# Performance work log

Measured on AMD Instinct MI355X. Metric: run time of the kernel, lower is better.

Reference implementation:

```python
import jax, jax.numpy as jnp
import numpy as np
from jax import lax

SMOOTH = 1e-06
SKEL_ITERS = 10  # thresh_width in the original soft_skeletonize


def _maxpool3(x):
    # 3x3 max pool, stride 1, padding 1 on NCHW
    return lax.reduce_window(
        x, -jnp.inf, lax.max,
        window_dimensions=(1, 1, 3, 3),
        window_strides=(1, 1, 1, 1),
        padding=((0, 0), (0, 0), (1, 1), (1, 1)))


def soft_skeletonize(x):
    def body(i, x):
        min_pool_x = -_maxpool3(-x)                      # 3x3 min-pool (erosion)
        contour = jax.nn.relu(_maxpool3(min_pool_x) - min_pool_x)
        return jax.nn.relu(x - contour)
    return lax.fori_loop(0, SKEL_ITERS, body, x)


def norm_intersection(center_line, vessel):
    B, C = center_line.shape[:2]
    clf = center_line.reshape(B, C, -1)
    vf = vessel.reshape(B, C, -1)
    intersection = jnp.sum(clf * vf, axis=-1)
    return (intersection + SMOOTH) / (jnp.sum(clf, axis=-1) + SMOOTH)


def setup_inputs() -> dict:
    key = jax.random.key(0)
    k1, k2 = jax.random.split(key)
    B, C, H, W = 32, 1, 512, 512
    pred = jax.random.uniform(k1, (B, C, H, W), dtype=jnp.float32)
    target = (jax.random.uniform(k2, (B, C, H, W), dtype=jnp.float32) > 0.85).astype(jnp.float32)
    return {"pred": pred, "target": target}


def reference(pred, target):
    cl_pred = soft_skeletonize(pred)
    target_skeleton = soft_skeletonize(target)
    iflat = norm_intersection(cl_pred, target)
    tflat = norm_intersection(target_skeleton, pred)
    intersection = jnp.sum(iflat * tflat)
    return 1.0 - 2.0 * intersection / jnp.sum(iflat + tflat)
```

## Files before the change

### kernel.cpp

```cpp
#include <hip/hip_runtime.h>
#include <hip/hip_fp16.h>
#include <math.h>

#define HH 512
#define WW 512
#define BB 32
#define CHUNK 32

typedef unsigned u32;

#define NEG_INF2 0xFC00FC00u
#define POS_INF2 0x7C007C00u

__device__ __forceinline__ u32 pkmin(u32 a, u32 b) {
    u32 r; asm("v_pk_min_f16 %0, %1, %2" : "=v"(r) : "v"(a), "v"(b)); return r;
}
__device__ __forceinline__ u32 pkmax(u32 a, u32 b) {
    u32 r; asm("v_pk_max_f16 %0, %1, %2" : "=v"(r) : "v"(a), "v"(b)); return r;
}
__device__ __forceinline__ u32 pksub(u32 a, u32 b) {
    u32 r; asm("v_pk_add_f16 %0, %1, %2 neg_lo:[0,1] neg_hi:[0,1]" : "=v"(r) : "v"(a), "v"(b)); return r;
}
__device__ __forceinline__ u32 min3p(u32 a, u32 b, u32 c) { return pkmin(pkmin(a, b), c); }
__device__ __forceinline__ u32 max3p(u32 a, u32 b, u32 c) { return pkmax(pkmax(a, b), c); }

__device__ __forceinline__ u32 shl1(u32 a, u32 b) {
    return __builtin_amdgcn_alignbit(b, a, 16);
}

union H2U { __half2 h; u32 u; };
__device__ __forceinline__ u32 f2toh2(float lo, float hi) {
    H2U t; t.h = __float22half2_rn(make_float2(lo, hi)); return t.u;
}
__device__ __forceinline__ float2 h2tof2(u32 v) {
    H2U t; t.u = v; return __half22float2(t.h);
}

template <int F32>
__device__ __forceinline__ void loadrow6(const float* __restrict__ imgF,
                                         const unsigned short* __restrict__ imgH,
                                         int R, int cm4, int c0, int cp4,
                                         bool isL, bool isR, u32* X) {
    const int Rc = R < 0 ? 0 : (R > HH - 1 ? HH - 1 : R);
    if (F32) {
        const float* rb = imgF + (size_t)Rc * WW;
        float4 v0 = *(const float4*)(rb + cm4);
        float4 v1 = *(const float4*)(rb + c0);
        float4 v2 = *(const float4*)(rb + cp4);
        X[0] = f2toh2(v0.x, v0.y); X[1] = f2toh2(v0.z, v0.w);
        X[2] = f2toh2(v1.x, v1.y); X[3] = f2toh2(v1.z, v1.w);
        X[4] = f2toh2(v2.x, v2.y); X[5] = f2toh2(v2.z, v2.w);
    } else {
        const unsigned short* rb = imgH + (size_t)Rc * WW;
        uint2 a = *(const uint2*)(rb + cm4);
        uint2 b = *(const uint2*)(rb + c0);
        uint2 c = *(const uint2*)(rb + cp4);
        X[0] = a.x; X[1] = a.y; X[2] = b.x; X[3] = b.y; X[4] = c.x; X[5] = c.y;
    }
    u32 fl = __builtin_amdgcn_perm(X[0], X[1], 0x05040100u);
    X[1] = isL ? fl : X[1];
    u32 fr = __builtin_amdgcn_perm(X[4], X[3], 0x07060302u);
    X[4] = isR ? fr : X[4];
}

template <int SRCF32, int FUSED>
__device__ __forceinline__ void rowstep(
    const float* __restrict__ imgF, const unsigned short* __restrict__ imgH,
    const float* __restrict__ cmp, unsigned short* __restrict__ outp,
    float& acc0, float& acc1,
    int R, int cm4, int gx0, int cp4, bool isL, bool isR, bool doStore,
    u32 (&X)[6], u32 (&XL)[6],
    u32 (&hm0o)[6], u32 (&hm0n)[6], u32 (&mn0p)[4],
    u32 (&hx0o)[4], u32 (&hx0n)[4],
    u32 (&x0o)[4], u32 (&x0n)[4],
    u32 (&hm1o)[4], u32 (&hm1n)[4], u32 (&mn1p)[2],
    u32 (&hx1o)[2], u32 (&hx1n)[2],
    u32 (&x1o)[2], u32 (&x1n)[2],
    const u32 (&mk)[8],
    float4& cqC, float4& cqL) {
    loadrow6<SRCF32>(imgF, imgH, R + 3, cm4, gx0, cp4, isL, isR, XL);

    float4 cmpCur;
    if (FUSED) {
        cmpCur = cqC;
        int Rc = R - 1;
        Rc = Rc < 0 ? 0 : (Rc > HH - 1 ? HH - 1 : Rc);
        cqL = *(const float4*)(cmp + (size_t)Rc * WW + gx0);
    }

    u32 L[7];
    L[0] = shl1(X[0], X[0]);
    #pragma unroll
    for (int j = 1; j <= 5; ++j) L[j] = shl1(X[j - 1], X[j]);
    L[6] = shl1(X[5], X[5]);
    u32 hm0c[6];
    #pragma unroll
    for (int j = 0; j < 6; ++j) hm0c[j] = min3p(L[j], X[j], L[j + 1]);

    u32 M[6];
    #pragma unroll
    for (int j = 0; j < 6; ++j) M[j] = min3p(hm0o[j], hm0n[j], hm0c[j]);
    if (!((unsigned)(R - 1) < HH)) {
        #pragma unroll
        for (int j = 0; j < 6; ++j) M[j] = NEG_INF2;
    }
    M[0] = pkmin(M[0], mk[0]); M[1] = pkmin(M[1], mk[1]);
    M[4] = pkmin(M[4], mk[2]); M[5] = pkmin(M[5], mk[3]);

    u32 ML[6];
    #pragma unroll
    for (int j = 1; j <= 5; ++j) ML[j] = shl1(M[j - 1], M[j]);
    u32 hx0c[4];
    #pragma unroll
    for (int j = 0; j < 4; ++j) hx0c[j] = max3p(ML[j + 1], M[j + 1], ML[j + 2]);

    u32 x1c[4];
    #pragma unroll
    for (int j = 0; j < 4; ++j) {
        u32 mp = max3p(hx0o[j], hx0n[j], hx0c[j]);
        u32 ct = pkmax(pksub(mp, mn0p[j]), 0u);
        x1c[j] = pkmax(pksub(x0o[j], ct), 0u);
    }
    if (!((unsigned)(R - 2) < HH)) {
        #pragma unroll
        for (int j = 0; j < 4; ++j) x1c[j] = POS_INF2;
    }
    x1c[0] = pkmax(x1c[0], mk[4]);
    x1c[3] = pkmax(x1c[3], mk[5]);

    #pragma unroll
    for (int j = 0; j < 6; ++j) hm0o[j] = hm0c[j];
    #pragma unroll
    for (int j = 0; j < 4; ++j) { mn0p[j] = M[j + 1]; hx0o[j] = hx0c[j]; x0o[j] = X[j + 1]; }

    u32 XL1[5];
    XL1[0] = shl1(x1c[0], x1c[0]);
    #pragma unroll
    for (int j = 1; j <= 3; ++j) XL1[j] = shl1(x1c[j - 1], x1c[j]);
    XL1[4] = shl1(x1c[3], x1c[3]);
    u32 hm1c[4];
    #pragma unroll
    for (int j = 0; j < 4; ++j) hm1c[j] = min3p(XL1[j], x1c[j], XL1[j + 1]);

    u32 M1[4];
    #pragma unroll
    for (int j = 0; j < 4; ++j) M1[j] = min3p(hm1o[j], hm1n[j], hm1c[j]);
    if (!((unsigned)(R - 3) < HH)) {
        #pragma unroll
        for (int j = 0; j < 4; ++j) M1[j] = NEG_INF2;
    }
    M1[0] = pkmin(M1[0], mk[6]);
    M1[3] = pkmin(M1[3], mk[7]);

    u32 M1s[4];
    #pragma unroll
    for (int j = 1; j <= 3; ++j) M1s[j] = shl1(M1[j - 1], M1[j]);
    u32 hx1c[2];
    hx1c[0] = max3p(M1s[1], M1[1], M1s[2]);
    hx1c[1] = max3p(M1s[2], M1[2], M1s[3]);

    if (doStore) {
        u32 o[2];
        #pragma unroll
        for (int k = 0; k < 2; ++k) {
            u32 mp = max3p(hx1o[k], hx1n[k], hx1c[k]);
            u32 ct = pkmax(pksub(mp, mn1p[k]), 0u);
            o[k] = pkmax(pksub(x1o[k], ct), 0u);
        }
        if (FUSED) {
            float2 f0 = h2tof2(o[0]);
            float2 f1 = h2tof2(o[1]);
            acc0 += f0.x * cmpCur.x + f0.y * cmpCur.y + f1.x * cmpCur.z + f1.y * cmpCur.w;
            acc1 += f0.x + f0.y + f1.x + f1.y;
        } else {
            uint2 ov;
            ov.x = o[0]; ov.y = o[1];
            *(uint2*)(outp + (size_t)(R - 4) * WW + gx0) = ov;
        }
    }

    #pragma unroll
    for (int j = 0; j < 4; ++j) hm1o[j] = hm1c[j];
    mn1p[0] = M1[1]; mn1p[1] = M1[2];
    hx1o[0] = hx1c[0]; hx1o[1] = hx1c[1];
    x1o[0] = x1c[1]; x1o[1] = x1c[2];
}

template <int SRCF32, int FUSED>
__global__ __launch_bounds__(256) void skel2h_t(const float* __restrict__ sfA,
                                                const float* __restrict__ sfB,
                                                const unsigned short* __restrict__ shA,
                                                const unsigned short* __restrict__ shB,
                                                const float* __restrict__ cmpA,
                                                const float* __restrict__ cmpB,
                                                unsigned short* __restrict__ dst,
                                                float* __restrict__ partials) {
    const int s = blockIdx.x * 64 + threadIdx.x;
    const int y0 = (blockIdx.y * 4 + threadIdx.y) * CHUNK;
    const int z = blockIdx.z;
    const float* imgF = nullptr;
    const unsigned short* imgH = nullptr;
    if (SRCF32) imgF = (z < BB) ? (sfA + (size_t)z * (HH * WW))
                                : (sfB + (size_t)(z - BB) * (HH * WW));
    else        imgH = (z < BB) ? (shA + (size_t)z * (HH * WW))
                                : (shB + (size_t)(z - BB) * (HH * WW));
    const float* cmp = nullptr;
    if (FUSED) cmp = (z < BB) ? (cmpA + (size_t)z * (HH * WW))
                              : (cmpB + (size_t)(z - BB) * (HH * WW));
    unsigned short* outp = FUSED ? nullptr : (dst + (size_t)z * (HH * WW));
    const int gx0 = 4 * s;
    const bool isL = (s == 0), isR = (s == 127);
    const int cm4 = isL ? 0 : gx0 - 4;
    const int cp4 = isR ? gx0 : gx0 + 4;

    u32 mk[8];
    mk[0] = isL ? 0xFC007C00u : POS_INF2;
    mk[1] = isL ? NEG_INF2    : POS_INF2;
    mk[2] = isR ? NEG_INF2    : POS_INF2;
    mk[3] = isR ? 0x7C00FC00u : POS_INF2;
    mk[4] = isL ? POS_INF2    : NEG_INF2;
    mk[5] = isR ? POS_INF2    : NEG_INF2;
    mk[6] = isL ? 0xFC007C00u : POS_INF2;
    mk[7] = isR ? 0x7C00FC00u : POS_INF2;

    u32 hm0a[6], hm0b[6], mn0p[4];
    u32 hx0a[4], hx0b[4], x0a[4], x0b[4];
    u32 hm1a[4], hm1b[4], mn1p[2];
    u32 hx1a[2], hx1b[2], x1a[2], x1b[2];
    u32 xs0[6], xs1[6], xs2[6], xs3[6];
    float4 cq0, cq1, cq2, cq3;

    #pragma unroll
    for (int j = 0; j < 6; ++j) { hm0a[j] = POS_INF2; hm0b[j] = POS_INF2; }
    #pragma unroll
    for (int j = 0; j < 4; ++j) {
        mn0p[j] = NEG_INF2; hx0a[j] = NEG_INF2; hx0b[j] = NEG_INF2;
        x0a[j] = POS_INF2; x0b[j] = POS_INF2;
        hm1a[j] = POS_INF2; hm1b[j] = POS_INF2;
    }
    #pragma unroll
    for (int k = 0; k < 2; ++k) {
        mn1p[k] = NEG_INF2; hx1a[k] = NEG_INF2; hx1b[k] = NEG_INF2;
        x1a[k] = POS_INF2; x1b[k] = POS_INF2;
    }
    cq0.x = cq0.y = cq0.z = cq0.w = 0.f;
    cq1 = cq0; cq2 = cq0; cq3 = cq0;

    float acc0 = 0.0f, acc1 = 0.0f;

    loadrow6<SRCF32>(imgF, imgH, y0 - 4, cm4, gx0, cp4, isL, isR, xs0);
    loadrow6<SRCF32>(imgF, imgH, y0 - 3, cm4, gx0, cp4, isL, isR, xs1);
    loadrow6<SRCF32>(imgF, imgH, y0 - 2, cm4, gx0, cp4, isL, isR, xs2);

    #pragma unroll 1
    for (int it = 0; it < (CHUNK + 8) / 4; ++it) {
        const int Rb = y0 - 4 + 4 * it;
        const bool doStore = (it >= 2);
        rowstep<SRCF32, FUSED>(imgF, imgH, cmp, outp, acc0, acc1,
            Rb + 0, cm4, gx0, cp4, isL, isR, doStore,
            xs0, xs3, hm0a, hm0b, mn0p, hx0a, hx0b, x0a, x0b,
            hm1a, hm1b, mn1p, hx1a, hx1b, x1a, x1b, mk, cq0, cq3);
        rowstep<SRCF32, FUSED>(imgF, imgH, cmp, outp, acc0, acc1,
            Rb + 1, cm4, gx0, cp4, isL, isR, doStore,
            xs1, xs0, hm0b, hm0a, mn0p, hx0b, hx0a, x0b, x0a,
            hm1b, hm1a, mn1p, hx1b, hx1a, x1b, x1a, mk, cq1, cq0);
        rowstep<SRCF32, FUSED>(imgF, imgH, cmp, outp, acc0, acc1,
            Rb + 2, cm4, gx0, cp4, isL, isR, doStore,
            xs2, xs1, hm0a, hm0b, mn0p, hx0a, hx0b, x0a, x0b,
            hm1a, hm1b, mn1p, hx1a, hx1b, x1a, x1b, mk, cq2, cq1);
        rowstep<SRCF32, FUSED>(imgF, imgH, cmp, outp, acc0, acc1,
            Rb + 3, cm4, gx0, cp4, isL, isR, doStore,
            xs3, xs2, hm0b, hm0a, mn0p, hx0b, hx0a, x0b, x0a,
            hm1b, hm1a, mn1p, hx1b, hx1a, x1b, x1a, mk, cq3, cq2);
    }

    if (FUSED) {
        for (int off = 32; off; off >>= 1) {
            acc0 += __shfl_down(acc0, off);
            acc1 += __shfl_down(acc1, off);
        }
        __shared__ float red[4][2];
        if (threadIdx.x == 0) { red[threadIdx.y][0] = acc0; red[threadIdx.y][1] = acc1; }
        __syncthreads();
        if (threadIdx.x == 0 && threadIdx.y == 0) {
            const int tile = blockIdx.x * gridDim.y + blockIdx.y;
            float* p = partials + ((size_t)z * 16 + tile) * 2;
            p[0] = red[0][0] + red[1][0] + red[2][0] + red[3][0];
            p[1] = red[0][1] + red[1][1] + red[2][1] + red[3][1];
        }
    }
}

__global__ __launch_bounds__(64) void finalize2(const float* __restrict__ partials,
                                                int ntiles,
                                                float* __restrict__ out) {
    const int b = threadIdx.x;
    float iflat = 0.f, tflat = 0.f;
    if (b < BB) {
        float v0 = 0.f, v1 = 0.f, v2 = 0.f, v3 = 0.f;
        for (int t = 0; t < ntiles; ++t) {
            v0 += partials[((size_t)b * 16 + t) * 2 + 0];
            v1 += partials[((size_t)b * 16 + t) * 2 + 1];
            v2 += partials[((size_t)(b + BB) * 16 + t) * 2 + 0];
            v3 += partials[((size_t)(b + BB) * 16 + t) * 2 + 1];
        }
        iflat = (v0 + 1e-6f) / (v1 + 1e-6f);
        tflat = (v2 + 1e-6f) / (v3 + 1e-6f);
    }
    float prod = iflat * tflat;
    float ssum = iflat + tflat;
    for (int off = 32; off; off >>= 1) {
        prod += __shfl_down(prod, off);
        ssum += __shfl_down(ssum, off);
    }
    if (threadIdx.x == 0) out[0] = 1.0f - 2.0f * prod / ssum;
}

extern "C" void kernel_launch(void* const* d_in, const int* in_sizes, int n_in,
                              void* d_out, int out_size, void* d_ws, size_t ws_size,
                              hipStream_t stream) {
    const float* pred = (const float*)d_in[0];
    const float* target = (const float*)d_in[1];
    float* out = (float*)d_out;
    char* ws = (char*)d_ws;
    const size_t N = (size_t)HH * WW;
    const size_t HALF = (size_t)BB * N;
    const size_t IMG16 = HALF * sizeof(unsigned short);

    dim3 block(64, 4);
    const int nby = HH / (CHUNK * 4);
    const int ntiles = 2 * nby;

    if (ws_size >= 4 * IMG16 + (1 << 16)) {
        unsigned short* A = (unsigned short*)ws;
        unsigned short* B = (unsigned short*)(ws + 2 * IMG16);
        float* partials = (float*)(ws + 4 * IMG16);
        dim3 grid(2, nby, 2 * BB);
        skel2h_t<1, 0><<<grid, block, 0, stream>>>(pred, target, nullptr, nullptr,
                                                   nullptr, nullptr, A, nullptr);
        skel2h_t<0, 0><<<grid, block, 0, stream>>>(nullptr, nullptr, A, A + HALF,
                                                   nullptr, nullptr, B, nullptr);
        skel2h_t<0, 0><<<grid, block, 0, stream>>>(nullptr, nullptr, B, B + HALF,
                                                   nullptr, nullptr, A, nullptr);
        skel2h_t<0, 0><<<grid, block, 0, stream>>>(nullptr, nullptr, A, A + HALF,
                                                   nullptr, nullptr, B, nullptr);
        skel2h_t<0, 1><<<grid, block, 0, stream>>>(nullptr, nullptr, B, B + HALF,
                                                   target, pred, nullptr, partials);
        finalize2<<<1, 64, 0, stream>>>(partials, ntiles, out);
    } else {
        unsigned short* b0 = (unsigned short*)ws;
        unsigned short* b1 = (unsigned short*)(ws + IMG16);
        float* partials = (float*)(ws + 2 * IMG16);
        dim3 grid(2, nby, BB);
        skel2h_t<1, 0><<<grid, block, 0, stream>>>(pred, pred, nullptr, nullptr,
                                                   nullptr, nullptr, b0, nullptr);
        skel2h_t<0, 0><<<grid, block, 0, stream>>>(nullptr, nullptr, b0, b0,
                                                   nullptr, nullptr, b1, nullptr);
        skel2h_t<0, 0><<<grid, block, 0, stream>>>(nullptr, nullptr, b1, b1,
                                                   nullptr, nullptr, b0, nullptr);
        skel2h_t<0, 0><<<grid, block, 0, stream>>>(nullptr, nullptr, b0, b0,
                                                   nullptr, nullptr, b1, nullptr);
        skel2h_t<0, 1><<<grid, block, 0, stream>>>(nullptr, nullptr, b1, b1,
                                                   target, target, nullptr, partials);
        skel2h_t<1, 0><<<grid, block, 0, stream>>>(target, target, nullptr, nullptr,
                                                   nullptr, nullptr, b0, nullptr);
        skel2h_t<0, 0><<<grid, block, 0, stream>>>(nullptr, nullptr, b0, b0,
                                                   nullptr, nullptr, b1, nullptr);
        skel2h_t<0, 0><<<grid, block, 0, stream>>>(nullptr, nullptr, b1, b1,
                                                   nullptr, nullptr, b0, nullptr);
        skel2h_t<0, 0><<<grid, block, 0, stream>>>(nullptr, nullptr, b0, b0,
                                                   nullptr, nullptr, b1, nullptr);
        skel2h_t<0, 1><<<grid, block, 0, stream>>>(nullptr, nullptr, b1, b1,
                                                   pred, pred, nullptr,
                                                   partials + (size_t)BB * 16 * 2);
        finalize2<<<1, 64, 0, stream>>>(partials, ntiles, out);
    }
}
```

Baseline: 143.4 us.

## Batch row loads four at a time in double-buffered groups for deeper prefetch

Replaces the per-row prefetch (one row ahead inside each rowstep) with a two-buffer scheme. Each iteration issues four row loads plus four compare-row loads, then processes the other buffer's four rows. This puts more memory requests in flight per wave to hide global load latency. The cost is more live registers (two 4x6 buffers plus float4 arrays), which may lower occupancy. The rowstep signature drops the x0n/x1n ping-pong arguments, and the handling of the clamped compare row at the edges changes.

```diff
diff --git a/kernel.cpp b/kernel.cpp
--- a/kernel.cpp
+++ b/kernel.cpp
@@ -63,31 +63,19 @@
     X[4] = isR ? fr : X[4];
 }
 
-template <int SRCF32, int FUSED>
+template <int FUSED>
 __device__ __forceinline__ void rowstep(
-    const float* __restrict__ imgF, const unsigned short* __restrict__ imgH,
-    const float* __restrict__ cmp, unsigned short* __restrict__ outp,
+    unsigned short* __restrict__ outp,
     float& acc0, float& acc1,
-    int R, int cm4, int gx0, int cp4, bool isL, bool isR, bool doStore,
-    u32 (&X)[6], u32 (&XL)[6],
+    int R, int gx0, bool isL, bool isR, bool doStore,
+    const u32 (&X)[6], const float4& cmpCur,
     u32 (&hm0o)[6], u32 (&hm0n)[6], u32 (&mn0p)[4],
     u32 (&hx0o)[4], u32 (&hx0n)[4],
-    u32 (&x0o)[4], u32 (&x0n)[4],
+    u32 (&x0o)[4],
     u32 (&hm1o)[4], u32 (&hm1n)[4], u32 (&mn1p)[2],
     u32 (&hx1o)[2], u32 (&hx1n)[2],
-    u32 (&x1o)[2], u32 (&x1n)[2],
-    const u32 (&mk)[8],
-    float4& cqC, float4& cqL) {
-    loadrow6<SRCF32>(imgF, imgH, R + 3, cm4, gx0, cp4, isL, isR, XL);
-
-    float4 cmpCur;
-    if (FUSED) {
-        cmpCur = cqC;
-        int Rc = R - 1;
-        Rc = Rc < 0 ? 0 : (Rc > HH - 1 ? HH - 1 : Rc);
-        cqL = *(const float4*)(cmp + (size_t)Rc * WW + gx0);
-    }
-
+    u32 (&x1o)[2],
+    const u32 (&mk)[8]) {
     u32 L[7];
     L[0] = shl1(X[0], X[0]);
     #pragma unroll
@@ -227,8 +215,7 @@
     u32 hx0a[4], hx0b[4], x0a[4], x0b[4];
     u32 hm1a[4], hm1b[4], mn1p[2];
     u32 hx1a[2], hx1b[2], x1a[2], x1b[2];
-    u32 xs0[6], xs1[6], xs2[6], xs3[6];
-    float4 cq0, cq1, cq2, cq3;
+    u32 bP[4][6], bN[4][6];
 
     #pragma unroll
     for (int j = 0; j < 6; ++j) { hm0a[j] = POS_INF2; hm0b[j] = POS_INF2; }
@@ -243,35 +230,72 @@
         mn1p[k] = NEG_INF2; hx1a[k] = NEG_INF2; hx1b[k] = NEG_INF2;
         x1a[k] = POS_INF2; x1b[k] = POS_INF2;
     }
-    cq0.x = cq0.y = cq0.z = cq0.w = 0.f;
-    cq1 = cq0; cq2 = cq0; cq3 = cq0;
 
     float acc0 = 0.0f, acc1 = 0.0f;
 
-    loadrow6<SRCF32>(imgF, imgH, y0 - 4, cm4, gx0, cp4, isL, isR, xs0);
-    loadrow6<SRCF32>(imgF, imgH, y0 - 3, cm4, gx0, cp4, isL, isR, xs1);
-    loadrow6<SRCF32>(imgF, imgH, y0 - 2, cm4, gx0, cp4, isL, isR, xs2);
+    loadrow6<SRCF32>(imgF, imgH, y0 - 4, cm4, gx0, cp4, isL, isR, bP[0]);
+    loadrow6<SRCF32>(imgF, imgH, y0 - 3, cm4, gx0, cp4, isL, isR, bP[1]);
+    loadrow6<SRCF32>(imgF, imgH, y0 - 2, cm4, gx0, cp4, isL, isR, bP[2]);
+    loadrow6<SRCF32>(imgF, imgH, y0 - 1, cm4, gx0, cp4, isL, isR, bP[3]);
 
     #pragma unroll 1
-    for (int it = 0; it < (CHUNK + 8) / 4; ++it) {
-        const int Rb = y0 - 4 + 4 * it;
-        const bool doStore = (it >= 2);
-        rowstep<SRCF32, FUSED>(imgF, imgH, cmp, outp, acc0, acc1,
-            Rb + 0, cm4, gx0, cp4, isL, isR, doStore,
-            xs0, xs3, hm0a, hm0b, mn0p, hx0a, hx0b, x0a, x0b,
-            hm1a, hm1b, mn1p, hx1a, hx1b, x1a, x1b, mk, cq0, cq3);
-        rowstep<SRCF32, FUSED>(imgF, imgH, cmp, outp, acc0, acc1,
-            Rb + 1, cm4, gx0, cp4, isL, isR, doStore,
-            xs1, xs0, hm0b, hm0a, mn0p, hx0b, hx0a, x0b, x0a,
-            hm1b, hm1a, mn1p, hx1b, hx1a, x1b, x1a, mk, cq1, cq0);
-        rowstep<SRCF32, FUSED>(imgF, imgH, cmp, outp, acc0, acc1,
-            Rb + 2, cm4, gx0, cp4, isL, isR, doStore,
-            xs2, xs1, hm0a, hm0b, mn0p, hx0a, hx0b, x0a, x0b,
-            hm1a, hm1b, mn1p, hx1a, hx1b, x1a, x1b, mk, cq2, cq1);
-        rowstep<SRCF32, FUSED>(imgF, imgH, cmp, outp, acc0, acc1,
-            Rb + 3, cm4, gx0, cp4, isL, isR, doStore,
-            xs3, xs2, hm0b, hm0a, mn0p, hx0b, hx0a, x0b, x0a,
-            hm1b, hm1a, mn1p, hx1b, hx1a, x1b, x1a, mk, cq3, cq2);
+    for (int it = 0; it < 5; ++it) {
+        const int base = y0 - 4 + 8 * it;
+        const bool st = (it >= 1);
+
+        loadrow6<SRCF32>(imgF, imgH, base + 4, cm4, gx0, cp4, isL, isR, bN[0]);
+        loadrow6<SRCF32>(imgF, imgH, base + 5, cm4, gx0, cp4, isL, isR, bN[1]);
+        loadrow6<SRCF32>(imgF, imgH, base + 6, cm4, gx0, cp4, isL, isR, bN[2]);
+        loadrow6<SRCF32>(imgF, imgH, base + 7, cm4, gx0, cp4, isL, isR, bN[3]);
+        float4 cA[4];
+        if (FUSED) {
+            cA[0].x = cA[0].y = cA[0].z = cA[0].w = 0.f;
+            cA[1] = cA[0]; cA[2] = cA[0]; cA[3] = cA[0];
+            if (st) {
+                cA[0] = *(const float4*)(cmp + (size_t)(base - 4) * WW + gx0);
+                cA[1] = *(const float4*)(cmp + (size_t)(base - 3) * WW + gx0);
+                cA[2] = *(const float4*)(cmp + (size_t)(base - 2) * WW + gx0);
+                cA[3] = *(const float4*)(cmp + (size_t)(base - 1) * WW + gx0);
+            }
+        } else {
+            cA[0].x = cA[0].y = cA[0].z = cA[0].w = 0.f;
+            cA[1] = cA[0]; cA[2] = cA[0]; cA[3] = cA[0];
+        }
+        rowstep<FUSED>(outp, acc0, acc1, base + 0, gx0, isL, isR, st, bP[0], cA[0],
+            hm0a, hm0b, mn0p, hx0a, hx0b, x0a, hm1a, hm1b, mn1p, hx1a, hx1b, x1a, mk);
+        rowstep<FUSED>(outp, acc0, acc1, base + 1, gx0, isL, isR, st, bP[1], cA[1],
+            hm0b, hm0a, mn0p, hx0b, hx0a, x0b, hm1b, hm1a, mn1p, hx1b, hx1a, x1b, mk);
+        rowstep<FUSED>(outp, acc0, acc1, base + 2, gx0, isL, isR, st, bP[2], cA[2],
+            hm0a, hm0b, mn0p, hx0a, hx0b, x0a, hm1a, hm1b, mn1p, hx1a, hx1b, x1a, mk);
+        rowstep<FUSED>(outp, acc0, acc1, base + 3, gx0, isL, isR, st, bP[3], cA[3],
+            hm0b, hm0a, mn0p, hx0b, hx0a, x0b, hm1b, hm1a, mn1p, hx1b, hx1a, x1b, mk);
+
+        loadrow6<SRCF32>(imgF, imgH, base + 8,  cm4, gx0, cp4, isL, isR, bP[0]);
+        loadrow6<SRCF32>(imgF, imgH, base + 9,  cm4, gx0, cp4, isL, isR, bP[1]);
+        loadrow6<SRCF32>(imgF, imgH, base + 10, cm4, gx0, cp4, isL, isR, bP[2]);
+        loadrow6<SRCF32>(imgF, imgH, base + 11, cm4, gx0, cp4, isL, isR, bP[3]);
+        float4 cB[4];
+        if (FUSED) {
+            cB[0].x = cB[0].y = cB[0].z = cB[0].w = 0.f;
+            cB[1] = cB[0]; cB[2] = cB[0]; cB[3] = cB[0];
+            if (st) {
+                cB[0] = *(const float4*)(cmp + (size_t)(base + 0) * WW + gx0);
+                cB[1] = *(const float4*)(cmp + (size_t)(base + 1) * WW + gx0);
+                cB[2] = *(const float4*)(cmp + (size_t)(base + 2) * WW + gx0);
+                cB[3] = *(const float4*)(cmp + (size_t)(base + 3) * WW + gx0);
+            }
+        } else {
+            cB[0].x = cB[0].y = cB[0].z = cB[0].w = 0.f;
+            cB[1] = cB[0]; cB[2] = cB[0]; cB[3] = cB[0];
+        }
+        rowstep<FUSED>(outp, acc0, acc1, base + 4, gx0, isL, isR, st, bN[0], cB[0],
+            hm0a, hm0b, mn0p, hx0a, hx0b, x0a, hm1a, hm1b, mn1p, hx1a, hx1b, x1a, mk);
+        rowstep<FUSED>(outp, acc0, acc1, base + 5, gx0, isL, isR, st, bN[1], cB[1],
+            hm0b, hm0a, mn0p, hx0b, hx0a, x0b, hm1b, hm1a, mn1p, hx1b, hx1a, x1b, mk);
+        rowstep<FUSED>(outp, acc0, acc1, base + 6, gx0, isL, isR, st, bN[2], cB[2],
+            hm0a, hm0b, mn0p, hx0a, hx0b, x0a, hm1a, hm1b, mn1p, hx1a, hx1b, x1a, mk);
+        rowstep<FUSED>(outp, acc0, acc1, base + 7, gx0, isL, isR, st, bN[3], cB[3],
+            hm0b, hm0a, mn0p, hx0b, hx0a, x0b, hm1b, hm1a, mn1p, hx1b, hx1a, x1b, mk);
     }
 
     if (FUSED) {
```

After: 143.8 us. Within noise of the previous version (+0.2%).

## Generalize skeleton kernel to fuse T iterations per launch, cutting launches

Applied to the files above, without the earlier changes.

Templates the row-streaming skeleton kernel on the number of fused iterations T, widening the horizontal halo to match and generalizing the per-stage boundary masks. The 10 iterations now run as 4+4+2 across three launches instead of 2 per launch across five, so the fp16 intermediate images make fewer round trips through global memory. In exchange each thread carries a larger halo and keeps more pipeline state in registers, adding redundant halo computation and possibly lowering occupancy or causing spills.

```diff
diff --git a/kernel.cpp b/kernel.cpp
--- a/kernel.cpp
+++ b/kernel.cpp
@@ -36,49 +36,51 @@
     H2U t; t.u = v; return __half22float2(t.h);
 }
 
-template <int F32>
-__device__ __forceinline__ void loadrow6(const float* __restrict__ imgF,
+template <int T, int F32>
+__device__ __forceinline__ void loadrowT(const float* __restrict__ imgF,
                                          const unsigned short* __restrict__ imgH,
-                                         int R, int cm4, int c0, int cp4,
-                                         bool isL, bool isR, u32* X) {
+                                         int R, const int (&pb)[T + 1],
+                                         const bool (&cXL)[2 * T + 2],
+                                         const bool (&cXR)[2 * T + 2],
+                                         u32 (&X)[2 * T + 2]) {
     const int Rc = R < 0 ? 0 : (R > HH - 1 ? HH - 1 : R);
     if (F32) {
         const float* rb = imgF + (size_t)Rc * WW;
-        float4 v0 = *(const float4*)(rb + cm4);
-        float4 v1 = *(const float4*)(rb + c0);
-        float4 v2 = *(const float4*)(rb + cp4);
-        X[0] = f2toh2(v0.x, v0.y); X[1] = f2toh2(v0.z, v0.w);
-        X[2] = f2toh2(v1.x, v1.y); X[3] = f2toh2(v1.z, v1.w);
-        X[4] = f2toh2(v2.x, v2.y); X[5] = f2toh2(v2.z, v2.w);
+        #pragma unroll
+        for (int m = 0; m <= T; ++m) {
+            float4 v = *(const float4*)(rb + 2 * pb[m]);
+            X[2 * m] = f2toh2(v.x, v.y); X[2 * m + 1] = f2toh2(v.z, v.w);
+        }
     } else {
         const unsigned short* rb = imgH + (size_t)Rc * WW;
-        uint2 a = *(const uint2*)(rb + cm4);
-        uint2 b = *(const uint2*)(rb + c0);
-        uint2 c = *(const uint2*)(rb + cp4);
-        X[0] = a.x; X[1] = a.y; X[2] = b.x; X[3] = b.y; X[4] = c.x; X[5] = c.y;
-    }
-    u32 fl = __builtin_amdgcn_perm(X[0], X[1], 0x05040100u);
-    X[1] = isL ? fl : X[1];
-    u32 fr = __builtin_amdgcn_perm(X[4], X[3], 0x07060302u);
-    X[4] = isR ? fr : X[4];
-}
-
-template <int SRCF32, int FUSED>
-__device__ __forceinline__ void rowstep(
+        #pragma unroll
+        for (int m = 0; m <= T; ++m) {
+            uint2 v = *(const uint2*)(rb + 2 * pb[m]);
+            X[2 * m] = v.x; X[2 * m + 1] = v.y;
+        }
+    }
+    #pragma unroll
+    for (int j = 0; j < T; ++j) X[j] = cXL[j] ? POS_INF2 : X[j];
+    #pragma unroll
+    for (int j = T + 2; j < 2 * T + 2; ++j) X[j] = cXR[j] ? POS_INF2 : X[j];
+}
+
+template <int T, int SRCF32, int FUSED>
+__device__ __forceinline__ void rowstepT(
     const float* __restrict__ imgF, const unsigned short* __restrict__ imgH,
     const float* __restrict__ cmp, unsigned short* __restrict__ outp,
     float& acc0, float& acc1,
-    int R, int cm4, int gx0, int cp4, bool isL, bool isR, bool doStore,
-    u32 (&X)[6], u32 (&XL)[6],
-    u32 (&hm0o)[6], u32 (&hm0n)[6], u32 (&mn0p)[4],
-    u32 (&hx0o)[4], u32 (&hx0n)[4],
-    u32 (&x0o)[4], u32 (&x0n)[4],
-    u32 (&hm1o)[4], u32 (&hm1n)[4], u32 (&mn1p)[2],
-    u32 (&hx1o)[2], u32 (&hx1n)[2],
-    u32 (&x1o)[2], u32 (&x1n)[2],
-    const u32 (&mk)[8],
+    int R, int gx0, bool doStore,
+    const int (&pb)[T + 1],
+    const bool (&cXL)[2 * T + 2], const bool (&cXR)[2 * T + 2],
+    const bool (&clv)[T + 2], const bool (&crv)[T + 3],
+    const u32 (&Xin)[2 * T + 2], u32 (&XL)[2 * T + 2],
+    u32 (&hmO)[T][2 * T + 2], u32 (&hmN)[T][2 * T + 2],
+    u32 (&mnp)[T][2 * T],
+    u32 (&hxO)[T][2 * T], u32 (&hxN)[T][2 * T],
+    u32 (&xO)[T][2 * T], u32 (&xN)[T][2 * T],
     float4& cqC, float4& cqL) {
-    loadrow6<SRCF32>(imgF, imgH, R + 3, cm4, gx0, cp4, isL, isR, XL);
+    loadrowT<T, SRCF32>(imgF, imgH, R + 3, pb, cXL, cXR, XL);
 
     float4 cmpCur;
     if (FUSED) {
@@ -88,113 +90,92 @@
         cqL = *(const float4*)(cmp + (size_t)Rc * WW + gx0);
     }
 
-    u32 L[7];
-    L[0] = shl1(X[0], X[0]);
-    #pragma unroll
-    for (int j = 1; j <= 5; ++j) L[j] = shl1(X[j - 1], X[j]);
-    L[6] = shl1(X[5], X[5]);
-    u32 hm0c[6];
-    #pragma unroll
-    for (int j = 0; j < 6; ++j) hm0c[j] = min3p(L[j], X[j], L[j + 1]);
-
-    u32 M[6];
-    #pragma unroll
-    for (int j = 0; j < 6; ++j) M[j] = min3p(hm0o[j], hm0n[j], hm0c[j]);
-    if (!((unsigned)(R - 1) < HH)) {
-        #pragma unroll
-        for (int j = 0; j < 6; ++j) M[j] = NEG_INF2;
-    }
-    M[0] = pkmin(M[0], mk[0]); M[1] = pkmin(M[1], mk[1]);
-    M[4] = pkmin(M[4], mk[2]); M[5] = pkmin(M[5], mk[3]);
-
-    u32 ML[6];
-    #pragma unroll
-    for (int j = 1; j <= 5; ++j) ML[j] = shl1(M[j - 1], M[j]);
-    u32 hx0c[4];
-    #pragma unroll
-    for (int j = 0; j < 4; ++j) hx0c[j] = max3p(ML[j + 1], M[j + 1], ML[j + 2]);
-
-    u32 x1c[4];
-    #pragma unroll
-    for (int j = 0; j < 4; ++j) {
-        u32 mp = max3p(hx0o[j], hx0n[j], hx0c[j]);
-        u32 ct = pkmax(pksub(mp, mn0p[j]), 0u);
-        x1c[j] = pkmax(pksub(x0o[j], ct), 0u);
-    }
-    if (!((unsigned)(R - 2) < HH)) {
-        #pragma unroll
-        for (int j = 0; j < 4; ++j) x1c[j] = POS_INF2;
-    }
-    x1c[0] = pkmax(x1c[0], mk[4]);
-    x1c[3] = pkmax(x1c[3], mk[5]);
-
-    #pragma unroll
-    for (int j = 0; j < 6; ++j) hm0o[j] = hm0c[j];
-    #pragma unroll
-    for (int j = 0; j < 4; ++j) { mn0p[j] = M[j + 1]; hx0o[j] = hx0c[j]; x0o[j] = X[j + 1]; }
-
-    u32 XL1[5];
-    XL1[0] = shl1(x1c[0], x1c[0]);
-    #pragma unroll
-    for (int j = 1; j <= 3; ++j) XL1[j] = shl1(x1c[j - 1], x1c[j]);
-    XL1[4] = shl1(x1c[3], x1c[3]);
-    u32 hm1c[4];
-    #pragma unroll
-    for (int j = 0; j < 4; ++j) hm1c[j] = min3p(XL1[j], x1c[j], XL1[j + 1]);
-
-    u32 M1[4];
-    #pragma unroll
-    for (int j = 0; j < 4; ++j) M1[j] = min3p(hm1o[j], hm1n[j], hm1c[j]);
-    if (!((unsigned)(R - 3) < HH)) {
-        #pragma unroll
-        for (int j = 0; j < 4; ++j) M1[j] = NEG_INF2;
-    }
-    M1[0] = pkmin(M1[0], mk[6]);
-    M1[3] = pkmin(M1[3], mk[7]);
-
-    u32 M1s[4];
-    #pragma unroll
-    for (int j = 1; j <= 3; ++j) M1s[j] = shl1(M1[j - 1], M1[j]);
-    u32 hx1c[2];
-    hx1c[0] = max3p(M1s[1], M1[1], M1s[2]);
-    hx1c[1] = max3p(M1s[2], M1[2], M1s[3]);
-
-    if (doStore) {
-        u32 o[2];
-        #pragma unroll
-        for (int k = 0; k < 2; ++k) {
-            u32 mp = max3p(hx1o[k], hx1n[k], hx1c[k]);
-            u32 ct = pkmax(pksub(mp, mn1p[k]), 0u);
-            o[k] = pkmax(pksub(x1o[k], ct), 0u);
-        }
-        if (FUSED) {
-            float2 f0 = h2tof2(o[0]);
-            float2 f1 = h2tof2(o[1]);
-            acc0 += f0.x * cmpCur.x + f0.y * cmpCur.y + f1.x * cmpCur.z + f1.y * cmpCur.w;
-            acc1 += f0.x + f0.y + f1.x + f1.y;
+    u32 cur[2 * T + 2];
+    #pragma unroll
+    for (int j = 0; j < 2 * T + 2; ++j) cur[j] = Xin[j];
+
+    #pragma unroll
+    for (int k = 0; k < T; ++k) {
+        const int WX = 2 + 2 * (T - k);
+        u32 L[2 * T + 3];
+        L[0] = shl1(cur[0], cur[0]);
+        #pragma unroll
+        for (int j = 1; j < WX; ++j) L[j] = shl1(cur[j - 1], cur[j]);
+        L[WX] = shl1(cur[WX - 1], cur[WX - 1]);
+        u32 hm[2 * T + 2];
+        #pragma unroll
+        for (int j = 0; j < WX; ++j) hm[j] = min3p(L[j], cur[j], L[j + 1]);
+        u32 M[2 * T + 2];
+        #pragma unroll
+        for (int j = 0; j < WX; ++j) M[j] = min3p(hmO[k][j], hmN[k][j], hm[j]);
+        if (!((unsigned)(R - (2 * k + 1)) < HH)) {
+            #pragma unroll
+            for (int j = 0; j < WX; ++j) M[j] = NEG_INF2;
+        }
+        #pragma unroll
+        for (int j = 0; j < WX; ++j) {
+            if (j < T - k)      M[j] = clv[(T - k) - j] ? NEG_INF2 : M[j];
+            if (j >= T - k + 2) M[j] = crv[j - (T - k)] ? NEG_INF2 : M[j];
+        }
+        u32 ML[2 * T + 2];
+        #pragma unroll
+        for (int j = 1; j < WX; ++j) ML[j] = shl1(M[j - 1], M[j]);
+        u32 hx[2 * T];
+        #pragma unroll
+        for (int j = 0; j < WX - 2; ++j) hx[j] = max3p(ML[j + 1], M[j + 1], ML[j + 2]);
+        u32 xn[2 * T];
+        #pragma unroll
+        for (int j = 0; j < WX - 2; ++j) {
+            u32 mp = max3p(hxO[k][j], hxN[k][j], hx[j]);
+            u32 ct = pkmax(pksub(mp, mnp[k][j]), 0u);
+            xn[j] = pkmax(pksub(xO[k][j], ct), 0u);
+        }
+        if (k < T - 1) {
+            if (!((unsigned)(R - (2 * k + 2)) < HH)) {
+                #pragma unroll
+                for (int j = 0; j < WX - 2; ++j) xn[j] = POS_INF2;
+            }
+        }
+        #pragma unroll
+        for (int j = 0; j < WX - 2; ++j) {
+            if (j <= T - k - 2) xn[j] = clv[(T - k) - j - 1] ? POS_INF2 : xn[j];
+            if (j >= T - k + 1) xn[j] = crv[j + 1 - (T - k)] ? POS_INF2 : xn[j];
+        }
+        #pragma unroll
+        for (int j = 0; j < WX; ++j) hmO[k][j] = hm[j];
+        #pragma unroll
+        for (int j = 0; j < WX - 2; ++j) {
+            mnp[k][j] = M[j + 1]; hxO[k][j] = hx[j]; xO[k][j] = cur[j + 1];
+        }
+        if (k == T - 1) {
+            if (doStore) {
+                if (FUSED) {
+                    float2 f0 = h2tof2(xn[0]);
+                    float2 f1 = h2tof2(xn[1]);
+                    acc0 += f0.x * cmpCur.x + f0.y * cmpCur.y + f1.x * cmpCur.z + f1.y * cmpCur.w;
+                    acc1 += f0.x + f0.y + f1.x + f1.y;
+                } else {
+                    uint2 ov; ov.x = xn[0]; ov.y = xn[1];
+                    *(uint2*)(outp + (size_t)(R - 2 * T) * WW + gx0) = ov;
+                }
+            }
         } else {
-            uint2 ov;
-            ov.x = o[0]; ov.y = o[1];
-            *(uint2*)(outp + (size_t)(R - 4) * WW + gx0) = ov;
-        }
-    }
-
-    #pragma unroll
-    for (int j = 0; j < 4; ++j) hm1o[j] = hm1c[j];
-    mn1p[0] = M1[1]; mn1p[1] = M1[2];
-    hx1o[0] = hx1c[0]; hx1o[1] = hx1c[1];
-    x1o[0] = x1c[1]; x1o[1] = x1c[2];
-}
-
-template <int SRCF32, int FUSED>
-__global__ __launch_bounds__(256) void skel2h_t(const float* __restrict__ sfA,
-                                                const float* __restrict__ sfB,
-                                                const unsigned short* __restrict__ shA,
-                                                const unsigned short* __restrict__ shB,
-                                                const float* __restrict__ cmpA,
-                                                const float* __restrict__ cmpB,
-                                                unsigned short* __restrict__ dst,
-                                                float* __restrict__ partials) {
+            #pragma unroll
+            for (int j = 0; j < WX - 2; ++j) cur[j] = xn[j];
+        }
+    }
+}
+
+template <int T, int SRCF32, int FUSED>
+__global__ __launch_bounds__(256) void skelT(const float* __restrict__ sfA,
+                                             const float* __restrict__ sfB,
+                                             const unsigned short* __restrict__ shA,
+                                             const unsigned short* __restrict__ shB,
+                                             const float* __restrict__ cmpA,
+                                             const float* __restrict__ cmpB,
+                                             unsigned short* __restrict__ dst,
+                                             float* __restrict__ partials) {
+    constexpr int NX = 2 * T + 2;
     const int s = blockIdx.x * 64 + threadIdx.x;
     const int y0 = (blockIdx.y * 4 + threadIdx.y) * CHUNK;
     const int z = blockIdx.z;
@@ -209,69 +190,70 @@
                               : (cmpB + (size_t)(z - BB) * (HH * WW));
     unsigned short* outp = FUSED ? nullptr : (dst + (size_t)z * (HH * WW));
     const int gx0 = 4 * s;
-    const bool isL = (s == 0), isR = (s == 127);
-    const int cm4 = isL ? 0 : gx0 - 4;
-    const int cp4 = isR ? gx0 : gx0 + 4;
-
-    u32 mk[8];
-    mk[0] = isL ? 0xFC007C00u : POS_INF2;
-    mk[1] = isL ? NEG_INF2    : POS_INF2;
-    mk[2] = isR ? NEG_INF2    : POS_INF2;
-    mk[3] = isR ? 0x7C00FC00u : POS_INF2;
-    mk[4] = isL ? POS_INF2    : NEG_INF2;
-    mk[5] = isR ? POS_INF2    : NEG_INF2;
-    mk[6] = isL ? 0xFC007C00u : POS_INF2;
-    mk[7] = isR ? 0x7C00FC00u : POS_INF2;
-
-    u32 hm0a[6], hm0b[6], mn0p[4];
-    u32 hx0a[4], hx0b[4], x0a[4], x0b[4];
-    u32 hm1a[4], hm1b[4], mn1p[2];
-    u32 hx1a[2], hx1b[2], x1a[2], x1b[2];
-    u32 xs0[6], xs1[6], xs2[6], xs3[6];
+    const int pl = 2 * s;
+
+    int pb[T + 1];
+    #pragma unroll
+    for (int m = 0; m <= T; ++m) {
+        int b = pl - T + 2 * m;
+        pb[m] = b < 0 ? 0 : (b > 254 ? 254 : b);
+    }
+    bool cXL[NX], cXR[NX];
+    #pragma unroll
+    for (int j = 0; j < NX; ++j) {
+        cXL[j] = (pl - T + j) < 0;
+        cXR[j] = (pl - T + j) > 255;
+    }
+    bool clv[T + 2], crv[T + 3];
+    #pragma unroll
+    for (int d = 0; d < T + 2; ++d) clv[d] = (pl < d);
+    #pragma unroll
+    for (int v = 0; v < T + 3; ++v) crv[v] = (pl > 255 - v);
+
+    u32 hmA[T][NX], hmB[T][NX];
+    u32 mnp[T][NX - 2];
+    u32 hxA[T][NX - 2], hxB[T][NX - 2];
+    u32 xA_[T][NX - 2], xB_[T][NX - 2];
+    #pragma unroll
+    for (int k = 0; k < T; ++k) {
+        const int WX = 2 + 2 * (T - k);
+        #pragma unroll
+        for (int j = 0; j < WX; ++j) { hmA[k][j] = POS_INF2; hmB[k][j] = POS_INF2; }
+        #pragma unroll
+        for (int j = 0; j < WX - 2; ++j) {
+            mnp[k][j] = NEG_INF2;
+            hxA[k][j] = NEG_INF2; hxB[k][j] = NEG_INF2;
+            xA_[k][j] = POS_INF2; xB_[k][j] = POS_INF2;
+        }
+    }
+
+    u32 xs0[NX], xs1[NX], xs2[NX], xs3[NX];
     float4 cq0, cq1, cq2, cq3;
-
-    #pragma unroll
-    for (int j = 0; j < 6; ++j) { hm0a[j] = POS_INF2; hm0b[j] = POS_INF2; }
-    #pragma unroll
-    for (int j = 0; j < 4; ++j) {
-        mn0p[j] = NEG_INF2; hx0a[j] = NEG_INF2; hx0b[j] = NEG_INF2;
-        x0a[j] = POS_INF2; x0b[j] = POS_INF2;
-        hm1a[j] = POS_INF2; hm1b[j] = POS_INF2;
-    }
-    #pragma unroll
-    for (int k = 0; k < 2; ++k) {
-        mn1p[k] = NEG_INF2; hx1a[k] = NEG_INF2; hx1b[k] = NEG_INF2;
-        x1a[k] = POS_INF2; x1b[k] = POS_INF2;
-    }
     cq0.x = cq0.y = cq0.z = cq0.w = 0.f;
     cq1 = cq0; cq2 = cq0; cq3 = cq0;
-
     float acc0 = 0.0f, acc1 = 0.0f;
 
-    loadrow6<SRCF32>(imgF, imgH, y0 - 4, cm4, gx0, cp4, isL, isR, xs0);
-    loadrow6<SRCF32>(imgF, imgH, y0 - 3, cm4, gx0, cp4, isL, isR, xs1);
-    loadrow6<SRCF32>(imgF, imgH, y0 - 2, cm4, gx0, cp4, isL, isR, xs2);
+    const int R0 = y0 - 2 * T;
+    loadrowT<T, SRCF32>(imgF, imgH, R0 + 0, pb, cXL, cXR, xs0);
+    loadrowT<T, SRCF32>(imgF, imgH, R0 + 1, pb, cXL, cXR, xs1);
+    loadrowT<T, SRCF32>(imgF, imgH, R0 + 2, pb, cXL, cXR, xs2);
 
     #pragma unroll 1
-    for (int it = 0; it < (CHUNK + 8) / 4; ++it) {
-        const int Rb = y0 - 4 + 4 * it;
-        const bool doStore = (it >= 2);
-        rowstep<SRCF32, FUSED>(imgF, imgH, cmp, outp, acc0, acc1,
-            Rb + 0, cm4, gx0, cp4, isL, isR, doStore,
-            xs0, xs3, hm0a, hm0b, mn0p, hx0a, hx0b, x0a, x0b,
-            hm1a, hm1b, mn1p, hx1a, hx1b, x1a, x1b, mk, cq0, cq3);
-        rowstep<SRCF32, FUSED>(imgF, imgH, cmp, outp, acc0, acc1,
-            Rb + 1, cm4, gx0, cp4, isL, isR, doStore,
-            xs1, xs0, hm0b, hm0a, mn0p, hx0b, hx0a, x0b, x0a,
-            hm1b, hm1a, mn1p, hx1b, hx1a, x1b, x1a, mk, cq1, cq0);
-        rowstep<SRCF32, FUSED>(imgF, imgH, cmp, outp, acc0, acc1,
-            Rb + 2, cm4, gx0, cp4, isL, isR, doStore,
-            xs2, xs1, hm0a, hm0b, mn0p, hx0a, hx0b, x0a, x0b,
-            hm1a, hm1b, mn1p, hx1a, hx1b, x1a, x1b, mk, cq2, cq1);
-        rowstep<SRCF32, FUSED>(imgF, imgH, cmp, outp, acc0, acc1,
-            Rb + 3, cm4, gx0, cp4, isL, isR, doStore,
-            xs3, xs2, hm0b, hm0a, mn0p, hx0b, hx0a, x0b, x0a,
-            hm1b, hm1a, mn1p, hx1b, hx1a, x1b, x1a, mk, cq3, cq2);
+    for (int it = 0; it < (CHUNK + 4 * T) / 4; ++it) {
+        const int Rb = R0 + 4 * it;
+        const bool st = (it >= T);
+        rowstepT<T, SRCF32, FUSED>(imgF, imgH, cmp, outp, acc0, acc1,
+            Rb + 0, gx0, st, pb, cXL, cXR, clv, crv, xs0, xs3,
+            hmA, hmB, mnp, hxA, hxB, xA_, xB_, cq0, cq3);
+        rowstepT<T, SRCF32, FUSED>(imgF, imgH, cmp, outp, acc0, acc1,
+            Rb + 1, gx0, st, pb, cXL, cXR, clv, crv, xs1, xs0,
+            hmB, hmA, mnp, hxB, hxA, xB_, xA_, cq1, cq0);
+        rowstepT<T, SRCF32, FUSED>(imgF, imgH, cmp, outp, acc0, acc1,
+            Rb + 2, gx0, st, pb, cXL, cXR, clv, crv, xs2, xs1,
+            hmA, hmB, mnp, hxA, hxB, xA_, xB_, cq2, cq1);
+        rowstepT<T, SRCF32, FUSED>(imgF, imgH, cmp, outp, acc0, acc1,
+            Rb + 3, gx0, st, pb, cXL, cXR, clv, crv, xs3, xs2,
+            hmB, hmA, mnp, hxB, hxA, xB_, xA_, cq3, cq2);
     }
 
     if (FUSED) {
@@ -336,15 +318,11 @@
         unsigned short* B = (unsigned short*)(ws + 2 * IMG16);
         float* partials = (float*)(ws + 4 * IMG16);
         dim3 grid(2, nby, 2 * BB);
-        skel2h_t<1, 0><<<grid, block, 0, stream>>>(pred, target, nullptr, nullptr,
+        skelT<4, 1, 0><<<grid, block, 0, stream>>>(pred, target, nullptr, nullptr,
                                                    nullptr, nullptr, A, nullptr);
-        skel2h_t<0, 0><<<grid, block, 0, stream>>>(nullptr, nullptr, A, A + HALF,
+        skelT<4, 0, 0><<<grid, block, 0, stream>>>(nullptr, nullptr, A, A + HALF,
                                                    nullptr, nullptr, B, nullptr);
-        skel2h_t<0, 0><<<grid, block, 0, stream>>>(nullptr, nullptr, B, B + HALF,
-                                                   nullptr, nullptr, A, nullptr);
-        skel2h_t<0, 0><<<grid, block, 0, stream>>>(nullptr, nullptr, A, A + HALF,
-                                                   nullptr, nullptr, B, nullptr);
-        skel2h_t<0, 1><<<grid, block, 0, stream>>>(nullptr, nullptr, B, B + HALF,
+        skelT<2, 0, 1><<<grid, block, 0, stream>>>(nullptr, nullptr, B, B + HALF,
                                                    target, pred, nullptr, partials);
         finalize2<<<1, 64, 0, stream>>>(partials, ntiles, out);
     } else {
@@ -352,25 +330,17 @@
         unsigned short* b1 = (unsigned short*)(ws + IMG16);
         float* partials = (float*)(ws + 2 * IMG16);
         dim3 grid(2, nby, BB);
-        skel2h_t<1, 0><<<grid, block, 0, stream>>>(pred, pred, nullptr, nullptr,
+        skelT<4, 1, 0><<<grid, block, 0, stream>>>(pred, pred, nullptr, nullptr,
                                                    nullptr, nullptr, b0, nullptr);
-        skel2h_t<0, 0><<<grid, block, 0, stream>>>(nullptr, nullptr, b0, b0,
+        skelT<4, 0, 0><<<grid, block, 0, stream>>>(nullptr, nullptr, b0, b0,
                                                    nullptr, nullptr, b1, nullptr);
-        skel2h_t<0, 0><<<grid, block, 0, stream>>>(nullptr, nullptr, b1, b1,
+        skelT<2, 0, 1><<<grid, block, 0, stream>>>(nullptr, nullptr, b1, b1,
+                                                   target, target, nullptr, partials);
+        skelT<4, 1, 0><<<grid, block, 0, stream>>>(target, target, nullptr, nullptr,
                                                    nullptr, nullptr, b0, nullptr);
-        skel2h_t<0, 0><<<grid, block, 0, stream>>>(nullptr, nullptr, b0, b0,
+        skelT<4, 0, 0><<<grid, block, 0, stream>>>(nullptr, nullptr, b0, b0,
                                                    nullptr, nullptr, b1, nullptr);
-        skel2h_t<0, 1><<<grid, block, 0, stream>>>(nullptr, nullptr, b1, b1,
-                                                   target, target, nullptr, partials);
-        skel2h_t<1, 0><<<grid, block, 0, stream>>>(target, target, nullptr, nullptr,
-                                                   nullptr, nullptr, b0, nullptr);
-        skel2h_t<0, 0><<<grid, block, 0, stream>>>(nullptr, nullptr, b0, b0,
-                                                   nullptr, nullptr, b1, nullptr);
-        skel2h_t<0, 0><<<grid, block, 0, stream>>>(nullptr, nullptr, b1, b1,
-                                                   nullptr, nullptr, b0, nullptr);
-        skel2h_t<0, 0><<<grid, block, 0, stream>>>(nullptr, nullptr, b0, b0,
-                                                   nullptr, nullptr, b1, nullptr);
-        skel2h_t<0, 1><<<grid, block, 0, stream>>>(nullptr, nullptr, b1, b1,
+        skelT<2, 0, 1><<<grid, block, 0, stream>>>(nullptr, nullptr, b1, b1,
                                                    pred, pred, nullptr,
                                                    partials + (size_t)BB * 16 * 2);
         finalize2<<<1, 64, 0, stream>>>(partials, ntiles, out);
```

Measured after the change: 229.2 us. 59.9% more time.
